# Performance work log

Measured on AMD Instinct MI355X. Metric: run time of the kernel, lower is better.

Reference implementation:

```python
import jax, jax.numpy as jnp
from jax import lax
import numpy as np

D_MODEL = 512
D_STATE = 16
D_CONV = 4
EXPAND = 2
D_INNER = EXPAND * D_MODEL  # 1024
DT_RANK = (D_MODEL + 15) // 16  # 32
FF_DIM = 1024
N_LAYERS = 2
B, L = 2, 2048


def setup_inputs() -> dict:
    key = jax.random.key(0)
    ks = jax.random.split(key, 16)
    s = 0.02
    x = jax.random.normal(ks[0], (B, L, D_MODEL), jnp.float32)
    in_proj_w = jax.random.normal(ks[1], (N_LAYERS, 2 * D_INNER, D_MODEL), jnp.float32) * s
    conv_w = jax.random.normal(ks[2], (N_LAYERS, D_INNER, D_CONV), jnp.float32) * 0.3
    conv_b = jax.random.normal(ks[3], (N_LAYERS, D_INNER), jnp.float32) * s
    x_proj_w = jax.random.normal(ks[4], (N_LAYERS, DT_RANK + 2 * D_STATE, D_INNER), jnp.float32) * s
    dt_proj_w = jax.random.normal(ks[5], (N_LAYERS, D_INNER, DT_RANK), jnp.float32) * s
    dt_proj_b = jax.random.normal(ks[6], (N_LAYERS, D_INNER), jnp.float32) * 0.5 - 4.0
    A_log = jnp.log(jnp.broadcast_to(jnp.arange(1, D_STATE + 1, dtype=jnp.float32), (N_LAYERS, D_INNER, D_STATE)))
    Dp = jnp.ones((N_LAYERS, D_INNER), jnp.float32)
    out_proj_w = jax.random.normal(ks[7], (N_LAYERS, D_MODEL, D_INNER), jnp.float32) * s
    mlp_w1 = jax.random.normal(ks[8], (FF_DIM, D_MODEL), jnp.float32) * s
    mlp_b1 = jnp.zeros((FF_DIM,), jnp.float32)
    mlp_w2 = jax.random.normal(ks[9], (D_MODEL, FF_DIM), jnp.float32) * s
    mlp_b2 = jnp.zeros((D_MODEL,), jnp.float32)
    return dict(x=x, in_proj_w=in_proj_w, conv_w=conv_w, conv_b=conv_b,
                x_proj_w=x_proj_w, dt_proj_w=dt_proj_w, dt_proj_b=dt_proj_b,
                A_log=A_log, Dp=Dp, out_proj_w=out_proj_w,
                mlp_w1=mlp_w1, mlp_b1=mlp_b1, mlp_w2=mlp_w2, mlp_b2=mlp_b2)


def _mamba_layer(x, ipw, cw, cb, xpw, dpw, dpb, Al, Dv, opw):
    # x: [B, L, d_model]
    b, l, _ = x.shape
    xz = jnp.einsum('bld,ed->ble', x, ipw)           # [B, L, 2*d_inner]
    xin, z = jnp.split(xz, 2, axis=-1)
    # causal depthwise conv1d (pad left d_conv-1)
    xc = jnp.transpose(xin, (0, 2, 1))               # [B, d_inner, L]
    xc = lax.conv_general_dilated(xc, cw[:, None, :], (1,), [(D_CONV - 1, 0)],
                                  feature_group_count=D_INNER)
    xin = jax.nn.silu(jnp.transpose(xc + cb[:, None], (0, 2, 1)))  # [B, L, d_inner]
    dbl = jnp.einsum('bld,ed->ble', xin, xpw)        # [B, L, dt_rank + 2*d_state]
    dt, Bm, Cm = jnp.split(dbl, [DT_RANK, DT_RANK + D_STATE], axis=-1)
    dt = jax.nn.softplus(jnp.einsum('blr,dr->bld', dt, dpw) + dpb)  # [B, L, d_inner]
    A = -jnp.exp(Al)                                  # [d_inner, d_state]
    dA = jnp.exp(dt[..., None] * A)                   # [B, L, d_inner, d_state]
    dBu = dt[..., None] * Bm[:, :, None, :] * xin[..., None]

    def step(h, inp):
        dA_t, dBu_t = inp
        h = dA_t * h + dBu_t
        return h, h

    h0 = jnp.zeros((b, D_INNER, D_STATE), x.dtype)
    _, hs = lax.scan(step, h0, (jnp.moveaxis(dA, 1, 0), jnp.moveaxis(dBu, 1, 0)))
    hs = jnp.moveaxis(hs, 0, 1)                       # [B, L, d_inner, d_state]
    y = jnp.einsum('blds,bls->bld', hs, Cm) + xin * Dv
    y = y * jax.nn.silu(z)
    return jnp.einsum('ble,de->bld', y, opw)


def reference(x, in_proj_w, conv_w, conv_b, x_proj_w, dt_proj_w, dt_proj_b,
              A_log, Dp, out_proj_w, mlp_w1, mlp_b1, mlp_w2, mlp_b2):
    residual = x
    for i in range(N_LAYERS):
        x = _mamba_layer(x, in_proj_w[i], conv_w[i], conv_b[i], x_proj_w[i],
                         dt_proj_w[i], dt_proj_b[i], A_log[i], Dp[i], out_proj_w[i])
    h = x + residual
    h = jax.nn.relu(jnp.einsum('bld,fd->blf', h, mlp_w1) + mlp_b1)  # dropout is identity in eval
    return jnp.einsum('blf,df->bld', h, mlp_w2) + mlp_b2
```

## Files before the change

### kernel.cpp

```cpp
#include <hip/hip_runtime.h>
#include <hip/hip_bf16.h>

#define BB 2
#define LL 2048
#define DMODEL 512
#define DSTATE 16
#define DINNER 1024
#define DTRANK 32
#define FFDIM 1024
#define MTOT (BB*LL)
#define SCL 64
#define NCC 32

typedef unsigned short u16;
typedef __attribute__((ext_vector_type(8))) short bf16x8;
typedef __attribute__((ext_vector_type(4))) float f32x4;

__device__ __forceinline__ float b2f(u16 u){
  unsigned v = ((unsigned)u) << 16; float f; __builtin_memcpy(&f, &v, 4); return f;
}
__device__ __forceinline__ u16 f2b(float f){
  unsigned u; __builtin_memcpy(&u, &f, 4);
  unsigned r = (u + 0x7FFFu + ((u >> 16) & 1u)) >> 16;
  return (u16)r;
}
__device__ __forceinline__ float siluf(float x){ return x / (1.f + __expf(-x)); }
__device__ __forceinline__ float softplusf(float v){
  return fmaxf(v, 0.f) + __logf(1.f + __expf(-fabsf(v)));
}

__device__ __forceinline__ float ldin(const void* p, size_t i, int bf){
  if (bf) return b2f(((const u16*)p)[i]);
  return ((const float*)p)[i];
}
__device__ __forceinline__ void stout(void* p, size_t i, int bf, float v){
  if (bf) ((u16*)p)[i] = f2b(v);
  else    ((float*)p)[i] = v;
}

__device__ __forceinline__ int getbf(const void* dp){
  return (*(const unsigned*)dp == 0x3F803F80u) ? 1 : 0;
}

template<int CVT>
__device__ __forceinline__ bf16x8 ld8(const void* P, size_t gi, int bf){
  if (!CVT || bf) return *(const bf16x8*)((const u16*)P + gi);
  float4 f0 = *(const float4*)((const float*)P + gi);
  float4 f1 = *(const float4*)((const float*)P + gi + 4);
  union { u16 u[8]; bf16x8 v; } t;
  t.u[0]=f2b(f0.x); t.u[1]=f2b(f0.y); t.u[2]=f2b(f0.z); t.u[3]=f2b(f0.w);
  t.u[4]=f2b(f1.x); t.u[5]=f2b(f1.y); t.u[6]=f2b(f1.z); t.u[7]=f2b(f1.w);
  return t.v;
}

#define CVT_IPW (2*2*DINNER*DMODEL)
#define CVT_XPW (2*64*DINNER)
#define CVT_DPW (2*DINNER*DTRANK)
#define CVT_OPW (2*DMODEL*DINNER)
#define CVT_W1  (FFDIM*DMODEL)
#define CVT_W2  (DMODEL*FFDIM)
#define CVT_CW  (2*DINNER*4)
#define CVT_CB  (2*DINNER)
#define CVT_TOT (CVT_IPW+CVT_XPW+CVT_DPW+CVT_OPW+CVT_W1+CVT_W2+CVT_CW+CVT_CB)
__global__ __launch_bounds__(256) void cvt_all_k(
    const void* __restrict__ ipw, const void* __restrict__ xpw,
    const void* __restrict__ dpw, const void* __restrict__ opw,
    const void* __restrict__ w1, const void* __restrict__ w2,
    const void* __restrict__ cw, const void* __restrict__ cb,
    u16* __restrict__ dst, const void* __restrict__ dprobe)
{
  const int bf = getbf(dprobe);
  size_t i4 = ((size_t)blockIdx.x * 256 + threadIdx.x) * 4;
  if (i4 >= CVT_TOT) return;
  const void* src; size_t off = i4;
  if      (off < CVT_IPW)                     { src = ipw; }
  else if ((off -= CVT_IPW) < CVT_XPW)        { src = xpw; }
  else if ((off -= CVT_XPW) < CVT_DPW)        { src = dpw; }
  else if ((off -= CVT_DPW) < CVT_OPW)        { src = opw; }
  else if ((off -= CVT_OPW) < CVT_W1)         { src = w1; }
  else if ((off -= CVT_W1)  < CVT_W2)         { src = w2; }
  else if ((off -= CVT_W2)  < CVT_CW)         { src = cw; }
  else     { off -= CVT_CW;                     src = cb; }
  ushort4 o;
  if (bf) {
    o = *(const ushort4*)((const u16*)src + off);
  } else {
    float4 f = *(const float4*)((const float*)src + off);
    o.x = f2b(f.x); o.y = f2b(f.y); o.z = f2b(f.z); o.w = f2b(f.w);
  }
  *(ushort4*)(dst + i4) = o;
}

template<int ACT, int CVA, int CVW, int CIN, int BM, int BN, int KB, int RESID>
__global__ __launch_bounds__(256) void gemm_mfma(
    const void* __restrict__ A, size_t aoff, int lda,
    const void* __restrict__ W, size_t woff,
    const void* __restrict__ bias, size_t boff,
    void* __restrict__ C, size_t coff, int ldc, int K,
    const void* __restrict__ xres, size_t xroff,
    const void* __restrict__ dprobe)
{
  const int bf = getbf(dprobe);
  constexpr int C8  = KB / 8;
  constexpr int TR  = 256 / C8;
  constexpr int ALD = BM / TR;
  constexpr int WLD = BN / TR;
  __shared__ __align__(16) u16 As[2][BM * KB];
  __shared__ __align__(16) u16 Ws[2][BN * KB];
  const int tid = threadIdx.x;
  const int row0 = blockIdx.y * BM, col0 = blockIdx.x * BN;
  const int wave = tid >> 6, lane = tid & 63;
  const int l15 = lane & 15, quad = lane >> 4;
  constexpr int WMT = (BM == 64) ? 1 : ((BN == 128) ? 4 : 2);
  const int mbase = (BM == 64) ? (wave * 16)
                  : ((BN == 128) ? (wave & 1) * 64 : wave * 32);
  const int nbase = (BM == 128 && BN == 128) ? (wave >> 1) * 64 : 0;

  const int rT = tid / C8, csw = tid % C8;
  const int scg = (KB == 32) ? (csw ^ ((rT >> 1) & 3)) : (csw ^ (rT & 7));
  const int lws = tid * 8;
  const size_t ab0 = aoff + (size_t)(row0 + rT) * lda + scg * 8;
  const size_t wb0 = woff + (size_t)(col0 + rT) * K   + scg * 8;

  f32x4 acc[WMT][4];
#pragma unroll
  for (int i = 0; i < WMT; i++)
#pragma unroll
    for (int j = 0; j < 4; j++) acc[i][j] = (f32x4){0.f,0.f,0.f,0.f};

  const int NT = K / KB;

  auto fchunk = [&](int r_, int g){
    return (KB == 32) ? (g ^ ((r_ >> 1) & 3)) : (g ^ (r_ & 7));
  };
  auto compute = [&](int cur_){
#pragma unroll
    for (int ks = 0; ks < KB / 32; ks++) {
      bf16x8 af_[WMT], bf_[4];
#pragma unroll
      for (int mt = 0; mt < WMT; mt++) {
        int r_ = mbase + mt * 16 + l15;
        af_[mt] = *(const bf16x8*)&As[cur_][r_ * KB + fchunk(r_, ks * 4 + quad) * 8];
      }
#pragma unroll
      for (int nt = 0; nt < 4; nt++) {
        int r_ = nbase + nt * 16 + l15;
        bf_[nt] = *(const bf16x8*)&Ws[cur_][r_ * KB + fchunk(r_, ks * 4 + quad) * 8];
      }
#pragma unroll
      for (int mt = 0; mt < WMT; mt++)
#pragma unroll
        for (int nt = 0; nt < 4; nt++)
          acc[mt][nt] = __builtin_amdgcn_mfma_f32_16x16x32_bf16(af_[mt], bf_[nt], acc[mt][nt], 0, 0, 0);
    }
  };

  bf16x8 ra0[ALD], rw0[WLD], ra1[ALD], rw1[WLD];

#define GLOAD(RA, RW, T) do { const int k1_ = (T) * KB;                        \
  _Pragma("unroll") for (int i = 0; i < ALD; i++)                              \
    RA[i] = ld8<CVA>(A, ab0 + k1_ + (size_t)i * TR * lda, bf);                 \
  _Pragma("unroll") for (int i = 0; i < WLD; i++)                              \
    RW[i] = ld8<CVW>(W, wb0 + k1_ + (size_t)i * TR * K, bf); } while (0)

#define GSTEP(RA, RW, T) do {                                                  \
  const int cur_ = (T) & 1;                                                    \
  _Pragma("unroll") for (int i = 0; i < ALD; i++)                              \
    *(bf16x8*)&As[cur_][lws + i * 2048] = RA[i];                               \
  _Pragma("unroll") for (int i = 0; i < WLD; i++)                              \
    *(bf16x8*)&Ws[cur_][lws + i * 2048] = RW[i];                               \
  if ((T) + 2 < NT) GLOAD(RA, RW, (T) + 2);                                    \
  __syncthreads();                                                             \
  compute(cur_);                                                               \
} while (0)

  GLOAD(ra0, rw0, 0);
  if (NT > 1) GLOAD(ra1, rw1, 1);
  int t = 0;
  for (; t + 1 < NT; t += 2) { GSTEP(ra0, rw0, t); GSTEP(ra1, rw1, t + 1); }
  if (t < NT) GSTEP(ra0, rw0, t);
#undef GLOAD
#undef GSTEP

#pragma unroll
  for (int nt = 0; nt < 4; nt++) {
    int c = col0 + nbase + nt * 16 + l15;
    float bv = bias ? ldin(bias, boff + c, bf) : 0.f;
#pragma unroll
    for (int mt = 0; mt < WMT; mt++) {
      int rb = row0 + mbase + mt * 16 + quad * 4;
#pragma unroll
      for (int r = 0; r < 4; r++) {
        float v = acc[mt][nt][r] + bv;
        if (ACT == 1) v = softplusf(v);
        if (ACT == 2) v = fmaxf(v, 0.f);
        size_t ci = (size_t)(rb + r) * ldc + c;
        if (RESID) v += ldin(xres, xroff + ci, bf);
        if (CIN) stout(C, coff + ci, bf, v);
        else     ((u16*)C)[coff + ci] = f2b(v);
      }
    }
  }
}

template<int FST>
__global__ __launch_bounds__(256) void conv_k(
    const u16* __restrict__ xz, const void* __restrict__ cw, size_t cwo,
    const void* __restrict__ cb, size_t cbo, u16* __restrict__ xc,
    const void* __restrict__ dprobe)
{
  if (FST) {
    const u16* cw16 = (const u16*)cw;
    const u16* cb16 = (const u16*)cb;
    int idx8 = (blockIdx.x * 256 + threadIdx.x) * 8;
    int d8 = idx8 & 1023;
    int row = idx8 >> 10;
    int lb = row & (LL - 1);
    bf16x8 cwv0 = *(const bf16x8*)&cw16[cwo + d8*4];
    bf16x8 cwv1 = *(const bf16x8*)&cw16[cwo + d8*4 + 8];
    bf16x8 cwv2 = *(const bf16x8*)&cw16[cwo + d8*4 + 16];
    bf16x8 cwv3 = *(const bf16x8*)&cw16[cwo + d8*4 + 24];
    bf16x8 cbv  = *(const bf16x8*)&cb16[cbo + d8];
    bf16x8 xv0 = (bf16x8){0,0,0,0,0,0,0,0}, xv1 = xv0, xv2 = xv0, xv3 = xv0;
    if (lb >= 3) xv0 = *(const bf16x8*)&xz[(size_t)(row - 3) * 2048 + d8];
    if (lb >= 2) xv1 = *(const bf16x8*)&xz[(size_t)(row - 2) * 2048 + d8];
    if (lb >= 1) xv2 = *(const bf16x8*)&xz[(size_t)(row - 1) * 2048 + d8];
    xv3 = *(const bf16x8*)&xz[(size_t)row * 2048 + d8];
    bf16x8 ov;
#pragma unroll
    for (int i = 0; i < 8; i++) {
      float acc = b2f((u16)cbv[i]);
      int c0 = i * 4;
      float w0 = b2f((u16)((c0 < 8) ? cwv0[c0 & 7] : (c0 < 16) ? cwv1[c0 & 7] : (c0 < 24) ? cwv2[c0 & 7] : cwv3[c0 & 7]));
      float w1_ = b2f((u16)(((c0+1) < 8) ? cwv0[(c0+1) & 7] : ((c0+1) < 16) ? cwv1[(c0+1) & 7] : ((c0+1) < 24) ? cwv2[(c0+1) & 7] : cwv3[(c0+1) & 7]));
      float w2_ = b2f((u16)(((c0+2) < 8) ? cwv0[(c0+2) & 7] : ((c0+2) < 16) ? cwv1[(c0+2) & 7] : ((c0+2) < 24) ? cwv2[(c0+2) & 7] : cwv3[(c0+2) & 7]));
      float w3_ = b2f((u16)(((c0+3) < 8) ? cwv0[(c0+3) & 7] : ((c0+3) < 16) ? cwv1[(c0+3) & 7] : ((c0+3) < 24) ? cwv2[(c0+3) & 7] : cwv3[(c0+3) & 7]));
      acc += w0 * b2f((u16)xv0[i]);
      acc += w1_ * b2f((u16)xv1[i]);
      acc += w2_ * b2f((u16)xv2[i]);
      acc += w3_ * b2f((u16)xv3[i]);
      ov[i] = (short)f2b(siluf(acc));
    }
    *(bf16x8*)&xc[idx8] = ov;
  } else {
    const int bf = getbf(dprobe);
    int idx = blockIdx.x * 256 + threadIdx.x;
    int d = idx & 1023;
    int row = idx >> 10;
    int lb = row & (LL - 1);
    float acc = ldin(cb, cbo + d, bf);
#pragma unroll
    for (int k = 0; k < 4; k++) {
      int lk = lb - 3 + k;
      if (lk >= 0) acc += ldin(cw, cwo + d*4 + k, bf) * b2f(xz[(size_t)(row - 3 + k) * 2048 + d]);
    }
    xc[idx] = f2b(siluf(acc));
  }
}

template<int CVW>
__global__ __launch_bounds__(256) void scan_A_k(
    const u16* __restrict__ xc,
    const u16* __restrict__ dbl,
    const void* __restrict__ dpwp, size_t dpwo,
    const void* __restrict__ dpbp, size_t dpbo,
    const void* __restrict__ Alog, size_t alo,
    float* __restrict__ Pc, float* __restrict__ Sc,
    const void* __restrict__ dprobe)
{
  const int bf = getbf(dprobe);
  int bid = blockIdx.x;
  int b = bid >> 9;
  int c = (bid >> 4) & (NCC - 1);
  int g = bid & 15;
  int t = threadIdx.x;
  int dl = t >> 2, sq = t & 3;
  int d0 = g * 64, d = d0 + dl;
  int rowb = b * LL + c * SCL;

  __shared__ __align__(16) u16 dts[64 * 64];
  __shared__ __align__(16) u16 us[64 * 64];
  __shared__ __align__(16) float Bs[64 * 20];
  u16* dbls = dts;
  u16* dpws = dts + 64 * 32;

  {
    int r = t >> 2, c8 = (t & 3) * 8;
    *(bf16x8*)&dbls[r * 32 + c8] =
        *(const bf16x8*)&dbl[(size_t)(rowb + r) * 64 + c8];
    *(bf16x8*)&dpws[r * 32 + c8] =
        ld8<CVW>(dpwp, dpwo + (size_t)(d0 + r) * DTRANK + c8, bf);
  }
#pragma unroll
  for (int p = 0; p < 2; p++) {
    int seg = p * 256 + t;
    int r = seg >> 3, c8 = (seg & 7) * 8;
    bf16x8 uv = *(const bf16x8*)&xc[(size_t)(rowb + r) * 1024 + d0 + c8];
    int coff = r >> 3, roff = r & 7;
#pragma unroll
    for (int i = 0; i < 8; i++) {
      int dd = c8 + i;
      us[dd * 64 + ((coff ^ (dd & 7)) << 3) + roff] = (u16)uv[i];
    }
  }
  if (t < 128) {
    int l = t >> 1, grp = t & 1;
    bf16x8 v = *(const bf16x8*)&dbl[(size_t)(rowb + l) * 64 + 32 + grp * 8];
    f32x4 f0 = {b2f((u16)v[0]), b2f((u16)v[1]), b2f((u16)v[2]), b2f((u16)v[3])};
    f32x4 f1 = {b2f((u16)v[4]), b2f((u16)v[5]), b2f((u16)v[6]), b2f((u16)v[7])};
    *(f32x4*)&Bs[l * 20 + grp * 8]     = f0;
    *(f32x4*)&Bs[l * 20 + grp * 8 + 4] = f1;
  }
  float Av[4];
#pragma unroll
  for (int j = 0; j < 4; j++)
    Av[j] = -__expf(ldin(Alog, alo + (size_t)d * DSTATE + sq * 4 + j, bf));
  __syncthreads();

  {
    int wv = t >> 6, lane = t & 63;
    int fl = lane & 15, qd = lane >> 4;
    bf16x8 afr  = *(const bf16x8*)&dbls[(wv * 16 + fl) * 32 + qd * 8];
    bf16x8 bfr0 = *(const bf16x8*)&dpws[(fl)      * 32 + qd * 8];
    bf16x8 bfr1 = *(const bf16x8*)&dpws[(16 + fl) * 32 + qd * 8];
    bf16x8 bfr2 = *(const bf16x8*)&dpws[(32 + fl) * 32 + qd * 8];
    bf16x8 bfr3 = *(const bf16x8*)&dpws[(48 + fl) * 32 + qd * 8];
    __syncthreads();
    f32x4 zz = {0.f, 0.f, 0.f, 0.f};
    f32x4 a0 = __builtin_amdgcn_mfma_f32_16x16x32_bf16(afr, bfr0, zz, 0, 0, 0);
    f32x4 a1 = __builtin_amdgcn_mfma_f32_16x16x32_bf16(afr, bfr1, zz, 0, 0, 0);
    f32x4 a2 = __builtin_amdgcn_mfma_f32_16x16x32_bf16(afr, bfr2, zz, 0, 0, 0);
    f32x4 a3 = __builtin_amdgcn_mfma_f32_16x16x32_bf16(afr, bfr3, zz, 0, 0, 0);
    int lc = wv * 2 + (qd >> 1);
    int off = (qd & 1) * 4;
#define DTWR(AN, NT) do {                                                      \
    int dd_ = (NT) * 16 + fl;                                                  \
    float bvv_ = ldin(dpbp, dpbo + d0 + dd_, bf);                              \
    ushort4 pk_;                                                               \
    pk_.x = f2b(softplusf(AN[0] + bvv_));                                      \
    pk_.y = f2b(softplusf(AN[1] + bvv_));                                      \
    pk_.z = f2b(softplusf(AN[2] + bvv_));                                      \
    pk_.w = f2b(softplusf(AN[3] + bvv_));                                      \
    *(ushort4*)&dts[dd_ * 64 + ((lc ^ (dd_ & 7)) << 3) + off] = pk_; } while (0)
    DTWR(a0, 0); DTWR(a1, 1); DTWR(a2, 2); DTWR(a3, 3);
#undef DTWR
  }
  __syncthreads();

  float h[4] = {0.f,0.f,0.f,0.f}, P[4] = {1.f,1.f,1.f,1.f};
  for (int cc = 0; cc < 8; cc++) {
    int base = dl * 64 + ((cc ^ (dl & 7)) << 3);
    bf16x8 dt8 = *(const bf16x8*)&dts[base];
    bf16x8 u8  = *(const bf16x8*)&us[base];
#pragma unroll
    for (int i = 0; i < 8; i++) {
      int l = cc * 8 + i;
      float dtv = b2f((u16)dt8[i]);
      float uv  = b2f((u16)u8[i]);
      float dtu = dtv * uv;
      f32x4 B4 = *(const f32x4*)&Bs[l * 20 + sq * 4];
#pragma unroll
      for (int j = 0; j < 4; j++) {
        float dA = __expf(dtv * Av[j]);
        h[j] = dA * h[j] + dtu * B4[j];
        P[j] *= dA;
      }
    }
  }
  size_t o = (((size_t)b * DINNER + d) * NCC + c) * DSTATE + sq * 4;
  *(f32x4*)&Pc[o] = (f32x4){P[0], P[1], P[2], P[3]};
  *(f32x4*)&Sc[o] = (f32x4){h[0], h[1], h[2], h[3]};
}

template<int CVW>
__global__ __launch_bounds__(256) void scan_C_k(
    u16* __restrict__ dtp, int sdt, const u16* __restrict__ xz,
    const u16* __restrict__ xc,
    const u16* __restrict__ dbl,
    const void* __restrict__ dpwp, size_t dpwo,
    const void* __restrict__ dpbp, size_t dpbo,
    const void* __restrict__ Alog, size_t alo,
    const void* __restrict__ Dpt, size_t dpo,
    const float* __restrict__ Pcp, const float* __restrict__ Scp,
    const void* __restrict__ dprobe)
{
  const int bf = getbf(dprobe);
  int bid = blockIdx.x;
  int b = bid >> 9;
  int c = (bid >> 4) & (NCC - 1);
  int g = bid & 15;
  int t = threadIdx.x;
  int dl = t >> 2, sq = t & 3;
  int d0 = g * 64, d = d0 + dl;
  int rowb = b * LL + c * SCL;

  __shared__ __align__(16) u16 dts[64 * 64];
  __shared__ __align__(16) u16 us[64 * 64];
  __shared__ __align__(16) u16 outs[64 * 64];
  __shared__ __align__(16) float BCs[64 * 36];
  u16* dbls = dts;
  u16* dpws = dts + 64 * 32;

  {
    int r = t >> 2, c8 = (t & 3) * 8;
    *(bf16x8*)&dbls[r * 32 + c8] =
        *(const bf16x8*)&dbl[(size_t)(rowb + r) * 64 + c8];
    *(bf16x8*)&dpws[r * 32 + c8] =
        ld8<CVW>(dpwp, dpwo + (size_t)(d0 + r) * DTRANK + c8, bf);
  }
#pragma unroll
  for (int p = 0; p < 2; p++) {
    int seg = p * 256 + t;
    int r = seg >> 3, c8 = (seg & 7) * 8;
    bf16x8 uv = *(const bf16x8*)&xc[(size_t)(rowb + r) * 1024 + d0 + c8];
    int coff = r >> 3, roff = r & 7;
#pragma unroll
    for (int i = 0; i < 8; i++) {
      int dd = c8 + i;
      us[dd * 64 + ((coff ^ (dd & 7)) << 3) + roff] = (u16)uv[i];
    }
  }
  {
    int l = t >> 2, grp = t & 3;
    bf16x8 v = *(const bf16x8*)&dbl[(size_t)(rowb + l) * 64 + 32 + grp * 8];
    f32x4 f0 = {b2f((u16)v[0]), b2f((u16)v[1]), b2f((u16)v[2]), b2f((u16)v[3])};
    f32x4 f1 = {b2f((u16)v[4]), b2f((u16)v[5]), b2f((u16)v[6]), b2f((u16)v[7])};
    *(f32x4*)&BCs[l * 36 + grp * 8]     = f0;
    *(f32x4*)&BCs[l * 36 + grp * 8 + 4] = f1;
  }
  float Av[4];
#pragma unroll
  for (int j = 0; j < 4; j++)
    Av[j] = -__expf(ldin(Alog, alo + (size_t)d * DSTATE + sq * 4 + j, bf));
  float Dv = ldin(Dpt, dpo + d, bf);
  float h[4] = {0.f, 0.f, 0.f, 0.f};
  {
    size_t ob = (((size_t)b * DINNER + d) * NCC) * DSTATE + sq * 4;
    for (int c2 = 0; c2 < c; c2++) {
      f32x4 P4 = *(const f32x4*)&Pcp[ob + (size_t)c2 * DSTATE];
      f32x4 S4 = *(const f32x4*)&Scp[ob + (size_t)c2 * DSTATE];
#pragma unroll
      for (int j = 0; j < 4; j++) h[j] = P4[j] * h[j] + S4[j];
    }
  }
  __syncthreads();

  {
    int wv = t >> 6, lane = t & 63;
    int fl = lane & 15, qd = lane >> 4;
    bf16x8 afr  = *(const bf16x8*)&dbls[(wv * 16 + fl) * 32 + qd * 8];
    bf16x8 bfr0 = *(const bf16x8*)&dpws[(fl)      * 32 + qd * 8];
    bf16x8 bfr1 = *(const bf16x8*)&dpws[(16 + fl) * 32 + qd * 8];
    bf16x8 bfr2 = *(const bf16x8*)&dpws[(32 + fl) * 32 + qd * 8];
    bf16x8 bfr3 = *(const bf16x8*)&dpws[(48 + fl) * 32 + qd * 8];
    __syncthreads();
    f32x4 zz = {0.f, 0.f, 0.f, 0.f};
    f32x4 a0 = __builtin_amdgcn_mfma_f32_16x16x32_bf16(afr, bfr0, zz, 0, 0, 0);
    f32x4 a1 = __builtin_amdgcn_mfma_f32_16x16x32_bf16(afr, bfr1, zz, 0, 0, 0);
    f32x4 a2 = __builtin_amdgcn_mfma_f32_16x16x32_bf16(afr, bfr2, zz, 0, 0, 0);
    f32x4 a3 = __builtin_amdgcn_mfma_f32_16x16x32_bf16(afr, bfr3, zz, 0, 0, 0);
    int lc = wv * 2 + (qd >> 1);
    int off = (qd & 1) * 4;
#define DTWR(AN, NT) do {                                                      \
    int dd_ = (NT) * 16 + fl;                                                  \
    float bvv_ = ldin(dpbp, dpbo + d0 + dd_, bf);                              \
    ushort4 pk_;                                                               \
    pk_.x = f2b(softplusf(AN[0] + bvv_));                                      \
    pk_.y = f2b(softplusf(AN[1] + bvv_));                                      \
    pk_.z = f2b(softplusf(AN[2] + bvv_));                                      \
    pk_.w = f2b(softplusf(AN[3] + bvv_));                                      \
    *(ushort4*)&dts[dd_ * 64 + ((lc ^ (dd_ & 7)) << 3) + off] = pk_; } while (0)
    DTWR(a0, 0); DTWR(a1, 1); DTWR(a2, 2); DTWR(a3, 3);
#undef DTWR
  }
  __syncthreads();

  for (int cc = 0; cc < 8; cc++) {
    int base = dl * 64 + ((cc ^ (dl & 7)) << 3);
    bf16x8 dt8 = *(const bf16x8*)&dts[base];
    bf16x8 u8  = *(const bf16x8*)&us[base];
#pragma unroll
    for (int i = 0; i < 8; i++) {
      int l = cc * 8 + i;
      float dtv = b2f((u16)dt8[i]);
      float uv  = b2f((u16)u8[i]);
      float dtu = dtv * uv;
      f32x4 B4 = *(const f32x4*)&BCs[l * 36 + sq * 4];
      f32x4 C4 = *(const f32x4*)&BCs[l * 36 + 16 + sq * 4];
      float y = 0.f;
#pragma unroll
      for (int j = 0; j < 4; j++) {
        float dA = __expf(dtv * Av[j]);
        h[j] = dA * h[j] + dtu * B4[j];
        y += h[j] * C4[j];
      }
      y += __shfl_xor(y, 1);
      y += __shfl_xor(y, 2);
      if (sq == 0) outs[l * 64 + dl] = f2b(y + uv * Dv);
    }
  }
  __syncthreads();
#pragma unroll
  for (int p = 0; p < 2; p++) {
    int seg = p * 256 + t;
    int r = seg >> 3, c8 = (seg & 7) * 8;
    bf16x8 yv = *(const bf16x8*)&outs[r * 64 + c8];
    bf16x8 zv = *(const bf16x8*)&xz[(size_t)(rowb + r) * 2048 + 1024 + d0 + c8];
    bf16x8 ov;
#pragma unroll
    for (int i = 0; i < 8; i++) {
      float z = b2f((u16)zv[i]);
      ov[i] = (short)f2b(b2f((u16)yv[i]) * siluf(z));
    }
    *(bf16x8*)&dtp[(size_t)(rowb + r) * sdt + d0 + c8] = ov;
  }
}

extern "C" void kernel_launch(void* const* d_in, const int* in_sizes, int n_in,
                              void* d_out, int out_size, void* d_ws, size_t ws_size,
                              hipStream_t stream) {
  const void* x_in = d_in[0];
  const void* ipw  = d_in[1];
  const void* cw   = d_in[2];
  const void* cb   = d_in[3];
  const void* xpw  = d_in[4];
  const void* dpw  = d_in[5];
  const void* dpb  = d_in[6];
  const void* Alog = d_in[7];
  const void* Dpt  = d_in[8];
  const void* opw  = d_in[9];
  const void* w1   = d_in[10];
  const void* b1   = d_in[11];
  const void* w2   = d_in[12];
  const void* b2   = d_in[13];

  const bool full = ws_size >= (size_t)64 * 1024 * 1024;
  const bool bfh = (in_sizes[1] == (int)(CVT_IPW * 2));

  if (full) {
    float* Pc = (float*)((char*)d_ws + 64);
    float* Sc = Pc + (size_t)BB*DINNER*NCC*DSTATE;
    u16* p = (u16*)(Sc + (size_t)BB*DINNER*NCC*DSTATE);
    u16* cvt0  = p;
    u16* ipw16 = p;  p += (size_t)CVT_IPW;
    u16* xpw16 = p;  p += (size_t)CVT_XPW;
    u16* dpw16 = p;  p += (size_t)CVT_DPW;
    u16* opw16 = p;  p += (size_t)CVT_OPW;
    u16* w116  = p;  p += (size_t)CVT_W1;
    u16* w216  = p;  p += (size_t)CVT_W2;
    u16* cw16  = p;  p += (size_t)CVT_CW;
    u16* cb16  = p;  p += (size_t)CVT_CB;
    u16* xz    = p;  p += (size_t)MTOT*2*DINNER;
    u16* xc    = p;  p += (size_t)MTOT*DINNER;
    u16* dty   = p;  p += (size_t)MTOT*DINNER;
    u16* dbl   = p;
    u16* bx = xc;
    u16* resid = xz;
    u16* hid = xz + (size_t)4*1024*1024;

    const u16* Wipw = bfh ? (const u16*)ipw : ipw16;
    const u16* Wxpw = bfh ? (const u16*)xpw : xpw16;
    const u16* Wdpw = bfh ? (const u16*)dpw : dpw16;
    const u16* Wopw = bfh ? (const u16*)opw : opw16;
    const u16* Ww1  = bfh ? (const u16*)w1  : w116;
    const u16* Ww2  = bfh ? (const u16*)w2  : w216;
    const u16* Wcw  = bfh ? (const u16*)cw  : cw16;
    const u16* Wcb  = bfh ? (const u16*)cb  : cb16;
    if (!bfh)
      cvt_all_k<<<(CVT_TOT/4 + 255)/256, 256, 0, stream>>>(
          ipw, xpw, dpw, opw, w1, w2, cw, cb, cvt0, Dpt);

    for (int layer = 0; layer < 2; layer++) {
      size_t ipw_o = (size_t)layer*2*DINNER*DMODEL;
      size_t cw_o  = (size_t)layer*DINNER*4,  cb_o = (size_t)layer*DINNER;
      size_t xpw_o = (size_t)layer*64*DINNER, dpw_o = (size_t)layer*DINNER*DTRANK;
      size_t dpb_o = (size_t)layer*DINNER,    al_o = (size_t)layer*DINNER*DSTATE;
      size_t dp_o  = (size_t)layer*DINNER,    opw_o = (size_t)layer*DMODEL*DINNER;
      if (layer == 0)
        gemm_mfma<0,1,0,0,128,128,32,0><<<dim3(16, 32), 256, 0, stream>>>(
            x_in, 0, DMODEL, Wipw, ipw_o, nullptr, 0, xz, 0, 2048, DMODEL,
            nullptr, 0, Dpt);
      else
        gemm_mfma<0,0,0,0,128,128,32,0><<<dim3(16, 32), 256, 0, stream>>>(
            bx, 0, DMODEL, Wipw, ipw_o, nullptr, 0, xz, 0, 2048, DMODEL,
            nullptr, 0, Dpt);
      conv_k<1><<<MTOT*DINNER/2048, 256, 0, stream>>>(
          xz, Wcw, cw_o, Wcb, cb_o, xc, Dpt);
      gemm_mfma<0,0,0,0,64,64,64,0><<<dim3(1, 64), 256, 0, stream>>>(
          xc, 0, DINNER, Wxpw, xpw_o, nullptr, 0, dbl, 0, 64, DINNER,
          nullptr, 0, Dpt);
      scan_A_k<0><<<BB*NCC*16, 256, 0, stream>>>(
          xc, dbl, Wdpw, dpw_o, dpb, dpb_o, Alog, al_o, Pc, Sc, Dpt);
      scan_C_k<0><<<BB*NCC*16, 256, 0, stream>>>(
          dty, 1024, xz, xc, dbl, Wdpw, dpw_o, dpb, dpb_o, Alog, al_o,
          Dpt, dp_o, Pc, Sc, Dpt);
      if (layer == 0)
        gemm_mfma<0,0,0,0,64,64,64,0><<<dim3(8, 64), 256, 0, stream>>>(
            dty, 0, 1024, Wopw, opw_o, nullptr, 0, bx, 0, DMODEL, DINNER,
            nullptr, 0, Dpt);
      else
        gemm_mfma<0,0,0,0,64,64,64,1><<<dim3(8, 64), 256, 0, stream>>>(
            dty, 0, 1024, Wopw, opw_o, nullptr, 0, resid, 0, DMODEL, DINNER,
            x_in, 0, Dpt);
    }
    gemm_mfma<2,0,0,0,64,64,64,0><<<dim3(16, 64), 256, 0, stream>>>(
        resid, 0, DMODEL, Ww1, 0, b1, 0, hid, 0, FFDIM, DMODEL,
        nullptr, 0, Dpt);
    gemm_mfma<0,0,0,1,64,64,64,0><<<dim3(8, 64), 256, 0, stream>>>(
        hid, 0, FFDIM, Ww2, 0, b2, 0, d_out, 0, DMODEL, FFDIM,
        nullptr, 0, Dpt);
  } else {
    float* Pc = (float*)((char*)d_ws + 64);
    float* Sc = Pc + (size_t)DINNER*NCC*DSTATE;
    u16* p = (u16*)(Sc + (size_t)DINNER*NCC*DSTATE);
    u16* xz  = p;  p += (size_t)LL*2*DINNER;
    u16* xc  = p;  p += (size_t)LL*DINNER;
    u16* bxF = p;  p += (size_t)MTOT*DMODEL;
    u16* dbl = p;
    u16* hid = xz + (size_t)2*1024*1024;

    for (int layer = 0; layer < 2; layer++) {
      size_t ipw_o = (size_t)layer*2*DINNER*DMODEL;
      size_t cw_o  = (size_t)layer*DINNER*4,  cb_o = (size_t)layer*DINNER;
      size_t xpw_o = (size_t)layer*64*DINNER, dpw_o = (size_t)layer*DINNER*DTRANK;
      size_t dpb_o = (size_t)layer*DINNER,    al_o = (size_t)layer*DINNER*DSTATE;
      size_t dp_o  = (size_t)layer*DINNER,    opw_o = (size_t)layer*DMODEL*DINNER;
      for (int b = 0; b < BB; b++) {
        size_t ro = (size_t)b * LL * DMODEL;
        if (layer == 0)
          gemm_mfma<0,1,1,0,128,128,32,0><<<dim3(16, 16), 256, 0, stream>>>(
              x_in, ro, DMODEL, ipw, ipw_o, nullptr, 0, xz, 0, 2048, DMODEL,
              nullptr, 0, Dpt);
        else
          gemm_mfma<0,0,1,0,128,128,32,0><<<dim3(16, 16), 256, 0, stream>>>(
              bxF, ro, DMODEL, ipw, ipw_o, nullptr, 0, xz, 0, 2048, DMODEL,
              nullptr, 0, Dpt);
        conv_k<0><<<LL*DINNER/256, 256, 0, stream>>>(xz, cw, cw_o, cb, cb_o, xc, Dpt);
        gemm_mfma<0,0,1,0,64,64,64,0><<<dim3(1, 32), 256, 0, stream>>>(
            xc, 0, DINNER, xpw, xpw_o, nullptr, 0, dbl, 0, 64, DINNER,
            nullptr, 0, Dpt);
        scan_A_k<1><<<NCC*16, 256, 0, stream>>>(
            xc, dbl, dpw, dpw_o, dpb, dpb_o, Alog, al_o, Pc, Sc, Dpt);
        scan_C_k<1><<<NCC*16, 256, 0, stream>>>(
            xz, 2048, xz, xc, dbl, dpw, dpw_o, dpb, dpb_o, Alog, al_o,
            Dpt, dp_o, Pc, Sc, Dpt);
        if (layer == 0)
          gemm_mfma<0,0,1,0,64,64,64,0><<<dim3(8, 32), 256, 0, stream>>>(
              xz, 0, 2048, opw, opw_o, nullptr, 0, bxF, ro, DMODEL, DINNER,
              nullptr, 0, Dpt);
        else
          gemm_mfma<0,0,1,0,64,64,64,1><<<dim3(8, 32), 256, 0, stream>>>(
              xz, 0, 2048, opw, opw_o, nullptr, 0, bxF, ro, DMODEL, DINNER,
              x_in, ro, Dpt);
      }
    }
    for (int b = 0; b < BB; b++) {
      size_t ro = (size_t)b * LL * DMODEL;
      gemm_mfma<2,0,1,0,64,64,64,0><<<dim3(16, 32), 256, 0, stream>>>(
          bxF, ro, DMODEL, w1, 0, b1, 0, hid, 0, FFDIM, DMODEL,
          nullptr, 0, Dpt);
      gemm_mfma<0,0,1,1,64,64,64,0><<<dim3(8, 32), 256, 0, stream>>>(
          hid, 0, FFDIM, w2, 0, b2, 0, d_out, ro, DMODEL, FFDIM,
          nullptr, 0, Dpt);
    }
  }
}
```

Before: 340.1 us.

## Add separate chunk-prefix scan kernel and retune GEMM tile sizes

```diff
diff --git a/kernel.cpp b/kernel.cpp
--- a/kernel.cpp
+++ b/kernel.cpp
@@ -372,6 +372,20 @@
   *(f32x4*)&Sc[o] = (f32x4){h[0], h[1], h[2], h[3]};
 }
 
+__global__ __launch_bounds__(256) void scan_B_k(
+    float* __restrict__ Pc, const float* __restrict__ Sc)
+{
+  int idx = blockIdx.x * 256 + threadIdx.x;
+  int bd = idx >> 4, s = idx & 15;
+  float h = 0.f;
+  for (int c = 0; c < NCC; c++) {
+    size_t o = ((size_t)bd * NCC + c) * DSTATE + s;
+    float P = Pc[o], S = Sc[o];
+    Pc[o] = h;
+    h = P * h + S;
+  }
+}
+
 template<int CVW>
 __global__ __launch_bounds__(256) void scan_C_k(
     u16* __restrict__ dtp, int sdt, const u16* __restrict__ xz,
@@ -380,8 +394,7 @@
     const void* __restrict__ dpwp, size_t dpwo,
     const void* __restrict__ dpbp, size_t dpbo,
     const void* __restrict__ Alog, size_t alo,
-    const void* __restrict__ Dpt, size_t dpo,
-    const float* __restrict__ Pcp, const float* __restrict__ Scp,
+    const void* __restrict__ Dpt, size_t dpo, const float* __restrict__ Hinit,
     const void* __restrict__ dprobe)
 {
   const int bf = getbf(dprobe);
@@ -433,16 +446,10 @@
   for (int j = 0; j < 4; j++)
     Av[j] = -__expf(ldin(Alog, alo + (size_t)d * DSTATE + sq * 4 + j, bf));
   float Dv = ldin(Dpt, dpo + d, bf);
-  float h[4] = {0.f, 0.f, 0.f, 0.f};
-  {
-    size_t ob = (((size_t)b * DINNER + d) * NCC) * DSTATE + sq * 4;
-    for (int c2 = 0; c2 < c; c2++) {
-      f32x4 P4 = *(const f32x4*)&Pcp[ob + (size_t)c2 * DSTATE];
-      f32x4 S4 = *(const f32x4*)&Scp[ob + (size_t)c2 * DSTATE];
-#pragma unroll
-      for (int j = 0; j < 4; j++) h[j] = P4[j] * h[j] + S4[j];
-    }
-  }
+  float h[4];
+  size_t o = (((size_t)b * DINNER + d) * NCC + c) * DSTATE + sq * 4;
+  f32x4 h4 = *(const f32x4*)&Hinit[o];
+  h[0] = h4[0]; h[1] = h4[1]; h[2] = h4[2]; h[3] = h4[3];
   __syncthreads();
 
   {
@@ -577,36 +584,37 @@
       size_t dpb_o = (size_t)layer*DINNER,    al_o = (size_t)layer*DINNER*DSTATE;
       size_t dp_o  = (size_t)layer*DINNER,    opw_o = (size_t)layer*DMODEL*DINNER;
       if (layer == 0)
-        gemm_mfma<0,1,0,0,128,128,32,0><<<dim3(16, 32), 256, 0, stream>>>(
+        gemm_mfma<0,1,0,0,128,64,32,0><<<dim3(32, 32), 256, 0, stream>>>(
             x_in, 0, DMODEL, Wipw, ipw_o, nullptr, 0, xz, 0, 2048, DMODEL,
             nullptr, 0, Dpt);
       else
-        gemm_mfma<0,0,0,0,128,128,32,0><<<dim3(16, 32), 256, 0, stream>>>(
+        gemm_mfma<0,0,0,0,128,64,32,0><<<dim3(32, 32), 256, 0, stream>>>(
             bx, 0, DMODEL, Wipw, ipw_o, nullptr, 0, xz, 0, 2048, DMODEL,
             nullptr, 0, Dpt);
       conv_k<1><<<MTOT*DINNER/2048, 256, 0, stream>>>(
           xz, Wcw, cw_o, Wcb, cb_o, xc, Dpt);
-      gemm_mfma<0,0,0,0,64,64,64,0><<<dim3(1, 64), 256, 0, stream>>>(
+      gemm_mfma<0,0,0,0,64,64,32,0><<<dim3(1, 64), 256, 0, stream>>>(
           xc, 0, DINNER, Wxpw, xpw_o, nullptr, 0, dbl, 0, 64, DINNER,
           nullptr, 0, Dpt);
       scan_A_k<0><<<BB*NCC*16, 256, 0, stream>>>(
           xc, dbl, Wdpw, dpw_o, dpb, dpb_o, Alog, al_o, Pc, Sc, Dpt);
+      scan_B_k<<<BB*64, 256, 0, stream>>>(Pc, Sc);
       scan_C_k<0><<<BB*NCC*16, 256, 0, stream>>>(
           dty, 1024, xz, xc, dbl, Wdpw, dpw_o, dpb, dpb_o, Alog, al_o,
-          Dpt, dp_o, Pc, Sc, Dpt);
+          Dpt, dp_o, Pc, Dpt);
       if (layer == 0)
-        gemm_mfma<0,0,0,0,64,64,64,0><<<dim3(8, 64), 256, 0, stream>>>(
+        gemm_mfma<0,0,0,0,64,64,32,0><<<dim3(8, 64), 256, 0, stream>>>(
             dty, 0, 1024, Wopw, opw_o, nullptr, 0, bx, 0, DMODEL, DINNER,
             nullptr, 0, Dpt);
       else
-        gemm_mfma<0,0,0,0,64,64,64,1><<<dim3(8, 64), 256, 0, stream>>>(
+        gemm_mfma<0,0,0,0,64,64,32,1><<<dim3(8, 64), 256, 0, stream>>>(
             dty, 0, 1024, Wopw, opw_o, nullptr, 0, resid, 0, DMODEL, DINNER,
             x_in, 0, Dpt);
     }
-    gemm_mfma<2,0,0,0,64,64,64,0><<<dim3(16, 64), 256, 0, stream>>>(
+    gemm_mfma<2,0,0,0,64,64,32,0><<<dim3(16, 64), 256, 0, stream>>>(
         resid, 0, DMODEL, Ww1, 0, b1, 0, hid, 0, FFDIM, DMODEL,
         nullptr, 0, Dpt);
-    gemm_mfma<0,0,0,1,64,64,64,0><<<dim3(8, 64), 256, 0, stream>>>(
+    gemm_mfma<0,0,0,1,64,64,32,0><<<dim3(8, 64), 256, 0, stream>>>(
         hid, 0, FFDIM, Ww2, 0, b2, 0, d_out, 0, DMODEL, FFDIM,
         nullptr, 0, Dpt);
   } else {
@@ -636,30 +644,31 @@
               bxF, ro, DMODEL, ipw, ipw_o, nullptr, 0, xz, 0, 2048, DMODEL,
               nullptr, 0, Dpt);
         conv_k<0><<<LL*DINNER/256, 256, 0, stream>>>(xz, cw, cw_o, cb, cb_o, xc, Dpt);
-        gemm_mfma<0,0,1,0,64,64,64,0><<<dim3(1, 32), 256, 0, stream>>>(
+        gemm_mfma<0,0,1,0,64,64,32,0><<<dim3(1, 32), 256, 0, stream>>>(
             xc, 0, DINNER, xpw, xpw_o, nullptr, 0, dbl, 0, 64, DINNER,
             nullptr, 0, Dpt);
         scan_A_k<1><<<NCC*16, 256, 0, stream>>>(
             xc, dbl, dpw, dpw_o, dpb, dpb_o, Alog, al_o, Pc, Sc, Dpt);
+        scan_B_k<<<64, 256, 0, stream>>>(Pc, Sc);
         scan_C_k<1><<<NCC*16, 256, 0, stream>>>(
             xz, 2048, xz, xc, dbl, dpw, dpw_o, dpb, dpb_o, Alog, al_o,
-            Dpt, dp_o, Pc, Sc, Dpt);
+            Dpt, dp_o, Pc, Dpt);
         if (layer == 0)
-          gemm_mfma<0,0,1,0,64,64,64,0><<<dim3(8, 32), 256, 0, stream>>>(
+          gemm_mfma<0,0,1,0,64,64,32,0><<<dim3(8, 32), 256, 0, stream>>>(
               xz, 0, 2048, opw, opw_o, nullptr, 0, bxF, ro, DMODEL, DINNER,
               nullptr, 0, Dpt);
         else
-          gemm_mfma<0,0,1,0,64,64,64,1><<<dim3(8, 32), 256, 0, stream>>>(
+          gemm_mfma<0,0,1,0,64,64,32,1><<<dim3(8, 32), 256, 0, stream>>>(
               xz, 0, 2048, opw, opw_o, nullptr, 0, bxF, ro, DMODEL, DINNER,
               x_in, ro, Dpt);
       }
     }
     for (int b = 0; b < BB; b++) {
       size_t ro = (size_t)b * LL * DMODEL;
-      gemm_mfma<2,0,1,0,64,64,64,0><<<dim3(16, 32), 256, 0, stream>>>(
+      gemm_mfma<2,0,1,0,64,64,32,0><<<dim3(16, 32), 256, 0, stream>>>(
           bxF, ro, DMODEL, w1, 0, b1, 0, hid, 0, FFDIM, DMODEL,
           nullptr, 0, Dpt);
-      gemm_mfma<0,0,1,1,64,64,64,0><<<dim3(8, 32), 256, 0, stream>>>(
+      gemm_mfma<0,0,1,1,64,64,32,0><<<dim3(8, 32), 256, 0, stream>>>(
           hid, 0, FFDIM, w2, 0, b2, 0, d_out, ro, DMODEL, FFDIM,
           nullptr, 0, Dpt);
     }
```

After: 340.9 us. No clear change (+0.2%).
